# Optimization experiments

Measured on AMD Instinct MI355X. Metric: run time of the kernel, lower is better.

The kernel has to match this reference:

```python
import jax, jax.numpy as jnp
import numpy as np

EPS = 1e-5  # BatchNorm eps

def gcn_conv(x, src, dst, deg, dinv, W, b):
    # PyG GCNConv: out = D^{-1/2}(A+I)D^{-1/2} X W + b
    N = x.shape[0]
    xw = x @ W                               # [N, F_out]
    norm = dinv[src] * dinv[dst]             # [E]
    agg = jax.ops.segment_sum(xw[src] * norm[:, None], dst, num_segments=N)
    agg = agg + xw * (1.0 / deg)[:, None]    # self-loop term: deg^-1/2 * deg^-1/2
    return agg + b

def bn(x, g, b, m, v):
    # inference-mode BatchNorm1d over features
    return (x - m) * jax.lax.rsqrt(v + EPS) * g + b

def setup_inputs() -> dict:
    key = jax.random.key(0)
    N, E, F_in, C = 100000, 1600000, 128, 16
    dims = [F_in, 64, 128, 64, 32, C]
    ks = jax.random.split(key, 64)
    inp = {}
    inp["x"] = jax.random.normal(ks[0], (N, F_in), dtype=jnp.float32)
    inp["edge_index"] = jax.random.randint(ks[1], (2, E), 0, N, dtype=jnp.int32)
    ki = 2
    for l in range(5):
        fi, fo = dims[l], dims[l + 1]
        scale = 1.0 / np.sqrt(fi)
        inp[f"w{l+1}"] = jax.random.normal(ks[ki], (fi, fo), dtype=jnp.float32) * scale; ki += 1
        inp[f"b{l+1}"] = jnp.zeros((fo,), dtype=jnp.float32)
    for l in range(4):  # BN params for layers 1..4
        fo = dims[l + 1]
        inp[f"g{l+1}"] = jnp.ones((fo,), dtype=jnp.float32)
        inp[f"be{l+1}"] = jnp.zeros((fo,), dtype=jnp.float32)
        inp[f"m{l+1}"] = jax.random.normal(ks[ki], (fo,), dtype=jnp.float32) * 0.1; ki += 1
        inp[f"v{l+1}"] = jax.random.uniform(ks[ki], (fo,), dtype=jnp.float32, minval=0.5, maxval=1.5); ki += 1
    return inp

def reference(x, edge_index,
              w1, b1, w2, b2, w3, b3, w4, b4, w5, b5,
              g1, be1, m1, v1, g2, be2, m2, v2,
              g3, be3, m3, v3, g4, be4, m4, v4):
    N = x.shape[0]
    src, dst = edge_index[0], edge_index[1]
    deg = jax.ops.segment_sum(jnp.ones(src.shape[0], x.dtype), dst, num_segments=N) + 1.0
    dinv = jax.lax.rsqrt(deg)
    h = jax.nn.relu(bn(gcn_conv(x, src, dst, deg, dinv, w1, b1), g1, be1, m1, v1))
    h = jax.nn.relu(bn(gcn_conv(h, src, dst, deg, dinv, w2, b2), g2, be2, m2, v2))
    h = jax.nn.relu(bn(gcn_conv(h, src, dst, deg, dinv, w3, b3), g3, be3, m3, v3))
    h = jax.nn.relu(bn(gcn_conv(h, src, dst, deg, dinv, w4, b4), g4, be4, m4, v4))
    return gcn_conv(h, src, dst, deg, dinv, w5, b5)
```

## Files before the change

kernel.cpp:

```cpp
#include <hip/hip_runtime.h>
#include <hip/hip_fp16.h>

#define BEPS 1e-5f
static constexpr int TPB = 256;
static constexpr int G_SC = 512;
static constexpr int BK_SHIFT = 8;
static constexpr int BK_NODES = 256;
static constexpr int KMAX = 512;
static constexpr int BK_SLACK = 2048;

union F4H8 { float4 f4; __half2 h2[4]; };

typedef _Float16 half8 __attribute__((ext_vector_type(8)));
typedef float floatx4 __attribute__((ext_vector_type(4)));


__global__ __launch_bounds__(TPB) void k_zero_int(int* __restrict__ p, int n) {
  int i = blockIdx.x * TPB + threadIdx.x;
  if (i < n) p[i] = 0;
}

__global__ __launch_bounds__(TPB) void k_hist(const int* __restrict__ dst,
                                              int* __restrict__ histG,
                                              int* __restrict__ btot,
                                              int E, int K, int chunk) {
  __shared__ int lh[KMAX];
  int g = blockIdx.x, t = threadIdx.x;
  for (int i = t; i < KMAX; i += TPB) lh[i] = 0;
  __syncthreads();
  int e0 = g * chunk, e1 = min(E, e0 + chunk);
  for (int e = e0 + t * 4; e < e1; e += TPB * 4) {
    if (e + 4 <= e1) {
      int4 d4 = *reinterpret_cast<const int4*>(dst + e);
      atomicAdd(&lh[d4.x >> BK_SHIFT], 1);
      atomicAdd(&lh[d4.y >> BK_SHIFT], 1);
      atomicAdd(&lh[d4.z >> BK_SHIFT], 1);
      atomicAdd(&lh[d4.w >> BK_SHIFT], 1);
    } else {
      for (int q = e; q < e1; ++q) atomicAdd(&lh[dst[q] >> BK_SHIFT], 1);
    }
  }
  __syncthreads();
  for (int i = t; i < K; i += TPB) {
    histG[i * G_SC + g] = lh[i];
    atomicAdd(&btot[i], lh[i]);
  }
}

__global__ __launch_bounds__(KMAX) void k_bbase(const int* __restrict__ btot,
                                                int* __restrict__ bbase, int K) {
  __shared__ int sh[KMAX];
  int t = threadIdx.x;
  int v = (t < K) ? btot[t] : 0;
  sh[t] = v;
  __syncthreads();
  for (int s = 1; s < KMAX; s <<= 1) {
    int x = sh[t];
    int y = (t >= s) ? sh[t - s] : 0;
    __syncthreads();
    sh[t] = x + y;
    __syncthreads();
  }
  if (t < K) bbase[t] = sh[t] - v;
  if (t == 0) bbase[K] = sh[K - 1];
}

__global__ __launch_bounds__(G_SC) void k_offs(const int* __restrict__ histG,
                                               const int* __restrict__ bbase,
                                               int* __restrict__ offs) {
  __shared__ int sh[G_SC];
  int b = blockIdx.x, t = threadIdx.x;
  int v = histG[b * G_SC + t];
  sh[t] = v;
  __syncthreads();
  for (int s = 1; s < G_SC; s <<= 1) {
    int x = sh[t];
    int y = (t >= s) ? sh[t - s] : 0;
    __syncthreads();
    sh[t] = x + y;
    __syncthreads();
  }
  offs[b * G_SC + t] = bbase[b] + sh[t] - v;
}

__global__ __launch_bounds__(TPB) void k_scatter(const int* __restrict__ src,
                                                 const int* __restrict__ dst,
                                                 const int* __restrict__ offs,
                                                 unsigned int* __restrict__ pairs,
                                                 int E, int K, int chunk) {
  __shared__ int cur[KMAX];
  int g = blockIdx.x, t = threadIdx.x;
  for (int i = t; i < K; i += TPB) cur[i] = offs[i * G_SC + g];
  __syncthreads();
  int e0 = g * chunk, e1 = min(E, e0 + chunk);
  for (int e = e0 + t * 4; e < e1; e += TPB * 4) {
    if (e + 4 <= e1) {
      int4 d4 = *reinterpret_cast<const int4*>(dst + e);
      int4 s4 = *reinterpret_cast<const int4*>(src + e);
      int p0 = atomicAdd(&cur[d4.x >> BK_SHIFT], 1);
      pairs[p0] = (unsigned int)s4.x | ((unsigned int)(d4.x & (BK_NODES - 1)) << 20);
      int p1 = atomicAdd(&cur[d4.y >> BK_SHIFT], 1);
      pairs[p1] = (unsigned int)s4.y | ((unsigned int)(d4.y & (BK_NODES - 1)) << 20);
      int p2 = atomicAdd(&cur[d4.z >> BK_SHIFT], 1);
      pairs[p2] = (unsigned int)s4.z | ((unsigned int)(d4.z & (BK_NODES - 1)) << 20);
      int p3 = atomicAdd(&cur[d4.w >> BK_SHIFT], 1);
      pairs[p3] = (unsigned int)s4.w | ((unsigned int)(d4.w & (BK_NODES - 1)) << 20);
    } else {
      for (int q = e; q < e1; ++q) {
        int d = dst[q];
        int pos = atomicAdd(&cur[d >> BK_SHIFT], 1);
        pairs[pos] = (unsigned int)src[q] | ((unsigned int)(d & (BK_NODES - 1)) << 20);
      }
    }
  }
}

__global__ __launch_bounds__(TPB) void k_bucket_sort(const unsigned int* __restrict__ pairs,
                                                     const int* __restrict__ bbase,
                                                     int* __restrict__ rowptr,
                                                     int* __restrict__ rowend,
                                                     int* __restrict__ colidx,
                                                     float* __restrict__ dinv,
                                                     int N, int E) {
  __shared__ int cur[BK_NODES];
  __shared__ int sh[BK_NODES];
  int b = blockIdx.x, t = threadIdx.x;
  int base = bbase[b], end = bbase[b + 1];
  int n0 = b << BK_SHIFT;
  int nNodes = min(BK_NODES, N - n0);
  cur[t] = 0;
  __syncthreads();
  for (int e = base + t; e < end; e += TPB) atomicAdd(&cur[pairs[e] >> 20], 1);
  __syncthreads();
  int v = cur[t];
  int pd = (v + 7) & ~7;
  sh[t] = pd;
  __syncthreads();
  for (int s = 1; s < TPB; s <<= 1) {
    int x = sh[t];
    int y = (t >= s) ? sh[t - s] : 0;
    __syncthreads();
    sh[t] = x + y;
    __syncthreads();
  }
  int Bb = (base + b * BK_SLACK + 7) & ~7;
  int start = Bb + (sh[t] - pd);
  if (t < nNodes) {
    rowptr[n0 + t] = start;
    rowend[n0 + t] = start + pd;
    dinv[n0 + t] = rsqrtf((float)(v + 1));
    for (int i = start + v; i < start + pd; ++i) colidx[i] = N;
  }
  __syncthreads();
  cur[t] = start;
  __syncthreads();
  for (int e = base + t; e < end; e += TPB) {
    unsigned int p = pairs[e];
    int pos = atomicAdd(&cur[p >> 20], 1);
    colidx[pos] = (int)(p & 0xFFFFFu);
  }
}

__device__ inline void packone(const float* __restrict__ W, _Float16* __restrict__ Wp,
                               int i, int FO) {
  int j = i & 7, lane = (i >> 3) & 63, tile = i >> 9;
  int nct = FO >> 4, ct = tile % nct, kch = tile / nct;
  int k = kch * 32 + ((lane >> 4) << 3) + j;
  int n = (ct << 4) + (lane & 15);
  Wp[i] = (_Float16)W[k * FO + n];
}

__global__ __launch_bounds__(TPB) void k_packAll(const float* w1, _Float16* p1,
                                                 const float* w2, _Float16* p2,
                                                 const float* w3, _Float16* p3,
                                                 const float* w4, _Float16* p4,
                                                 const float* w5, _Float16* p5,
                                                 __half* bufA, int N) {
  int i = blockIdx.x * TPB + threadIdx.x;
  if (i < 8192) packone(w1, p1, i, 64);
  else if (i < 16384) packone(w2, p2, i - 8192, 128);
  else if (i < 24576) packone(w3, p3, i - 16384, 64);
  else if (i < 26624) packone(w4, p4, i - 24576, 32);
  else if (i < 27136) packone(w5, p5, i - 26624, 16);
  else if (i < 27144) {
    float4 z = {0.f, 0.f, 0.f, 0.f};
    reinterpret_cast<float4*>(bufA + (size_t)64 * N)[i - 27136] = z;
  }
}

template <int FI, int FO, int EPI, bool F32IN>
__global__ __launch_bounds__(TPB) void k_mgemm(const void* __restrict__ hin,
                                               const _Float16* __restrict__ Wp,
                                               const float* __restrict__ dinv,
                                               const float* __restrict__ bias,
                                               const float* __restrict__ g,
                                               const float* __restrict__ be,
                                               const float* __restrict__ m,
                                               const float* __restrict__ v,
                                               __half* __restrict__ out, int N) {
  constexpr int NCT = FO / 16;
  constexpr int NKC = FI / 32;
  __shared__ float4 Wsh[NKC * NCT * 64];
  for (int i = threadIdx.x; i < NKC * NCT * 64; i += TPB)
    Wsh[i] = reinterpret_cast<const float4*>(Wp)[i];
  __syncthreads();

  int lane = threadIdx.x & 63;
  int wv = threadIdx.x >> 6;
  int quad = lane >> 4;
  int rowBase = blockIdx.x * 64 + wv * 16;
  int rA = min(rowBase + (lane & 15), N - 1);

  floatx4 acc[NCT];
#pragma unroll
  for (int ct = 0; ct < NCT; ++ct) acc[ct] = (floatx4){0.f, 0.f, 0.f, 0.f};

#pragma unroll
  for (int kch = 0; kch < NKC; ++kch) {
    half8 a;
    if constexpr (F32IN) {
      const float4* xp = reinterpret_cast<const float4*>(hin);
      size_t idx = ((size_t)rA * FI + kch * 32 + quad * 8) >> 2;
      float4 fa = xp[idx], fb = xp[idx + 1];
      a[0] = (_Float16)fa.x; a[1] = (_Float16)fa.y; a[2] = (_Float16)fa.z; a[3] = (_Float16)fa.w;
      a[4] = (_Float16)fb.x; a[5] = (_Float16)fb.y; a[6] = (_Float16)fb.z; a[7] = (_Float16)fb.w;
    } else {
      union { float4 f4; half8 h8; } ua;
      ua.f4 = reinterpret_cast<const float4*>(hin)[((size_t)rA * FI + kch * 32 + quad * 8) >> 3];
      a = ua.h8;
    }
#pragma unroll
    for (int ct = 0; ct < NCT; ++ct) {
      union { float4 f4; half8 h8; } ub;
      ub.f4 = Wsh[(kch * NCT + ct) * 64 + lane];
      acc[ct] = __builtin_amdgcn_mfma_f32_16x16x32_f16(a, ub.h8, acc[ct], 0, 0, 0);
    }
  }

  int r0 = rowBase + quad * 4;
  float dv[4];
#pragma unroll
  for (int reg = 0; reg < 4; ++reg) dv[reg] = (r0 + reg < N) ? dinv[r0 + reg] : 0.f;
#pragma unroll
  for (int ct = 0; ct < NCT; ++ct) {
    int col = ct * 16 + (lane & 15);
#pragma unroll
    for (int reg = 0; reg < 4; ++reg) {
      int r = r0 + reg;
      out[(size_t)r * FO + col] = __float2half(acc[ct][reg] * dv[reg]);
    }
  }
  (void)bias; (void)g; (void)be; (void)m; (void)v;
}

template <int DO_BN>
__device__ inline void agg_gather64(const float4* __restrict__ in16,
                                    const int* __restrict__ rowptr,
                                    const int* __restrict__ rowend,
                                    const int* __restrict__ colidx,
                                    const float* __restrict__ dinv,
                                    const float* __restrict__ b_,
                                    const float* __restrict__ g_,
                                    const float* __restrict__ be_,
                                    const float* __restrict__ m_,
                                    const float* __restrict__ v_,
                                    int node, int quad, int N, half8 afr[2]) {
  bool valid = node < N;
  int rd = valid ? node : N;
  int e0 = valid ? rowptr[node] : 0;
  int e1 = valid ? rowend[node] : 0;
  float acc[2][8];
#pragma unroll
  for (int kch = 0; kch < 2; ++kch) {
    F4H8 u;
    u.f4 = in16[(size_t)rd * 8 + kch * 4 + quad];
#pragma unroll
    for (int i = 0; i < 4; ++i) {
      float2 t2 = __half22float2(u.h2[i]);
      acc[kch][2 * i] = t2.x;
      acc[kch][2 * i + 1] = t2.y;
    }
  }
  for (int e = e0; e < e1; e += 4) {
    int4 c = *reinterpret_cast<const int4*>(colidx + e);
#pragma unroll
    for (int kch = 0; kch < 2; ++kch) {
      int g = kch * 4 + quad;
      F4H8 u0, u1, u2, u3;
      u0.f4 = in16[(size_t)c.x * 8 + g];
      u1.f4 = in16[(size_t)c.y * 8 + g];
      u2.f4 = in16[(size_t)c.z * 8 + g];
      u3.f4 = in16[(size_t)c.w * 8 + g];
#pragma unroll
      for (int i = 0; i < 4; ++i) {
        float2 a = __half22float2(u0.h2[i]), b = __half22float2(u1.h2[i]);
        float2 cc = __half22float2(u2.h2[i]), d = __half22float2(u3.h2[i]);
        acc[kch][2 * i] += (a.x + b.x) + (cc.x + d.x);
        acc[kch][2 * i + 1] += (a.y + b.y) + (cc.y + d.y);
      }
    }
  }
  float dv = valid ? dinv[node] : 0.f;
#pragma unroll
  for (int kch = 0; kch < 2; ++kch) {
    int f0 = kch * 32 + quad * 8;
#pragma unroll
    for (int j = 0; j < 8; ++j) {
      float val = acc[kch][j] * dv;
      if (DO_BN) {
        int f = f0 + j;
        float sc = g_[f] * rsqrtf(v_[f] + BEPS);
        val = fmaxf((val + b_[f] - m_[f]) * sc + be_[f], 0.f);
      }
      afr[kch][j] = (_Float16)val;
    }
  }
}

__global__ __launch_bounds__(TPB) void k_aggemm23(const __half* __restrict__ hin,
                                                  const int* __restrict__ rowptr,
                                                  const int* __restrict__ rowend,
                                                  const int* __restrict__ colidx,
                                                  const _Float16* __restrict__ W2p,
                                                  const _Float16* __restrict__ W3p,
                                                  const float* __restrict__ dinv,
                                                  const float* __restrict__ b2,
                                                  const float* __restrict__ g2,
                                                  const float* __restrict__ be2,
                                                  const float* __restrict__ m2,
                                                  const float* __restrict__ v2,
                                                  __half* __restrict__ out, int N) {
  __shared__ float4 W2s[2 * 8 * 64];
  __shared__ float4 W3s[4 * 4 * 64];
  __shared__ _Float16 tr[4 * 16 * 136];
  for (int i = threadIdx.x; i < 1024; i += TPB) W2s[i] = reinterpret_cast<const float4*>(W2p)[i];
  for (int i = threadIdx.x; i < 1024; i += TPB) W3s[i] = reinterpret_cast<const float4*>(W3p)[i];
  __syncthreads();

  int lane = threadIdx.x & 63;
  int wv = threadIdx.x >> 6;
  int quad = lane >> 4;
  int m = lane & 15;
  int rowBase = blockIdx.x * 64 + wv * 16;

  half8 afr[2];
  agg_gather64<0>(reinterpret_cast<const float4*>(hin), rowptr, rowend, colidx, dinv,
                  nullptr, nullptr, nullptr, nullptr, nullptr, rowBase + m, quad, N, afr);

  floatx4 acc1[8];
#pragma unroll
  for (int ct = 0; ct < 8; ++ct) acc1[ct] = (floatx4){0.f, 0.f, 0.f, 0.f};
#pragma unroll
  for (int kch = 0; kch < 2; ++kch) {
#pragma unroll
    for (int ct = 0; ct < 8; ++ct) {
      union { float4 f4; half8 h8; } ub;
      ub.f4 = W2s[(kch * 8 + ct) * 64 + lane];
      acc1[ct] = __builtin_amdgcn_mfma_f32_16x16x32_f16(afr[kch], ub.h8, acc1[ct], 0, 0, 0);
    }
  }
  _Float16* mytr = tr + wv * 16 * 136;
#pragma unroll
  for (int ct = 0; ct < 8; ++ct) {
    int col = ct * 16 + m;
    float sc = g2[col] * rsqrtf(v2[col] + BEPS);
    float bb = b2[col] - m2[col];
    float ee = be2[col];
#pragma unroll
    for (int reg = 0; reg < 4; ++reg) {
      int r = quad * 4 + reg;
      mytr[r * 136 + col] = (_Float16)fmaxf((acc1[ct][reg] + bb) * sc + ee, 0.f);
    }
  }
  floatx4 acc2[4];
#pragma unroll
  for (int ct = 0; ct < 4; ++ct) acc2[ct] = (floatx4){0.f, 0.f, 0.f, 0.f};
#pragma unroll
  for (int kch = 0; kch < 4; ++kch) {
    half8 a2 = *reinterpret_cast<const half8*>(&mytr[m * 136 + kch * 32 + quad * 8]);
#pragma unroll
    for (int ct = 0; ct < 4; ++ct) {
      union { float4 f4; half8 h8; } ub;
      ub.f4 = W3s[(kch * 4 + ct) * 64 + lane];
      acc2[ct] = __builtin_amdgcn_mfma_f32_16x16x32_f16(a2, ub.h8, acc2[ct], 0, 0, 0);
    }
  }
  int r0 = rowBase + quad * 4;
  float dv[4];
#pragma unroll
  for (int reg = 0; reg < 4; ++reg) dv[reg] = (r0 + reg < N) ? dinv[r0 + reg] : 0.f;
#pragma unroll
  for (int ct = 0; ct < 4; ++ct) {
    int col = ct * 16 + m;
#pragma unroll
    for (int reg = 0; reg < 4; ++reg) {
      int r = r0 + reg;
      out[(size_t)r * 64 + col] = __float2half(acc2[ct][reg] * dv[reg]);
    }
  }
}

template <int FO>
__global__ __launch_bounds__(TPB) void k_aggemm64(const __half* __restrict__ hin,
                                                  const int* __restrict__ rowptr,
                                                  const int* __restrict__ rowend,
                                                  const int* __restrict__ colidx,
                                                  const _Float16* __restrict__ Wp,
                                                  const float* __restrict__ dinv,
                                                  const float* __restrict__ b_,
                                                  const float* __restrict__ g_,
                                                  const float* __restrict__ be_,
                                                  const float* __restrict__ m_,
                                                  const float* __restrict__ v_,
                                                  __half* __restrict__ out, int N) {
  constexpr int NCT = FO / 16;
  __shared__ float4 Wsh[2 * NCT * 64];
  for (int i = threadIdx.x; i < 2 * NCT * 64; i += TPB)
    Wsh[i] = reinterpret_cast<const float4*>(Wp)[i];
  __syncthreads();

  int lane = threadIdx.x & 63;
  int wv = threadIdx.x >> 6;
  int quad = lane >> 4;
  int m = lane & 15;
  int rowBase = blockIdx.x * 64 + wv * 16;

  half8 afr[2];
  agg_gather64<1>(reinterpret_cast<const float4*>(hin), rowptr, rowend, colidx, dinv,
                  b_, g_, be_, m_, v_, rowBase + m, quad, N, afr);

  floatx4 acc[NCT];
#pragma unroll
  for (int ct = 0; ct < NCT; ++ct) acc[ct] = (floatx4){0.f, 0.f, 0.f, 0.f};
#pragma unroll
  for (int kch = 0; kch < 2; ++kch) {
#pragma unroll
    for (int ct = 0; ct < NCT; ++ct) {
      union { float4 f4; half8 h8; } ub;
      ub.f4 = Wsh[(kch * NCT + ct) * 64 + lane];
      acc[ct] = __builtin_amdgcn_mfma_f32_16x16x32_f16(afr[kch], ub.h8, acc[ct], 0, 0, 0);
    }
  }
  int r0 = rowBase + quad * 4;
  float dv[4];
#pragma unroll
  for (int reg = 0; reg < 4; ++reg) dv[reg] = (r0 + reg < N) ? dinv[r0 + reg] : 0.f;
#pragma unroll
  for (int ct = 0; ct < NCT; ++ct) {
    int col = ct * 16 + m;
#pragma unroll
    for (int reg = 0; reg < 4; ++reg) {
      int r = r0 + reg;
      out[(size_t)r * FO + col] = __float2half(acc[ct][reg] * dv[reg]);
    }
  }
}

__global__ __launch_bounds__(TPB) void k_aggemm5(const __half* __restrict__ hin,
                                                 const int* __restrict__ rowptr,
                                                 const int* __restrict__ rowend,
                                                 const int* __restrict__ colidx,
                                                 const _Float16* __restrict__ Wp,
                                                 const float* __restrict__ dinv,
                                                 const float* __restrict__ b_,
                                                 const float* __restrict__ g_,
                                                 const float* __restrict__ be_,
                                                 const float* __restrict__ m_,
                                                 const float* __restrict__ v_,
                                                 __half* __restrict__ out, int N) {
  __shared__ float4 Wsh[64];
  if (threadIdx.x < 64) Wsh[threadIdx.x] = reinterpret_cast<const float4*>(Wp)[threadIdx.x];
  __syncthreads();

  int lane = threadIdx.x & 63;
  int wv = threadIdx.x >> 6;
  int quad = lane >> 4;
  int m = lane & 15;
  int rowBase = blockIdx.x * 64 + wv * 16;
  int node = rowBase + m;
  bool valid = node < N;
  int rd = valid ? node : N;
  int e0 = valid ? rowptr[node] : 0;
  int e1 = valid ? rowend[node] : 0;
  const float4* in16 = reinterpret_cast<const float4*>(hin);

  float acc[8];
  {
    F4H8 u;
    u.f4 = in16[(size_t)rd * 4 + quad];
#pragma unroll
    for (int i = 0; i < 4; ++i) {
      float2 t2 = __half22float2(u.h2[i]);
      acc[2 * i] = t2.x;
      acc[2 * i + 1] = t2.y;
    }
  }
  for (int e = e0; e < e1; e += 4) {
    int4 c = *reinterpret_cast<const int4*>(colidx + e);
    F4H8 u0, u1, u2, u3;
    u0.f4 = in16[(size_t)c.x * 4 + quad];
    u1.f4 = in16[(size_t)c.y * 4 + quad];
    u2.f4 = in16[(size_t)c.z * 4 + quad];
    u3.f4 = in16[(size_t)c.w * 4 + quad];
#pragma unroll
    for (int i = 0; i < 4; ++i) {
      float2 a = __half22float2(u0.h2[i]), b = __half22float2(u1.h2[i]);
      float2 cc = __half22float2(u2.h2[i]), d = __half22float2(u3.h2[i]);
      acc[2 * i] += (a.x + b.x) + (cc.x + d.x);
      acc[2 * i + 1] += (a.y + b.y) + (cc.y + d.y);
    }
  }
  float dvn = valid ? dinv[node] : 0.f;
  half8 afr;
#pragma unroll
  for (int j = 0; j < 8; ++j) {
    int f = quad * 8 + j;
    float sc = g_[f] * rsqrtf(v_[f] + BEPS);
    float val = fmaxf((acc[j] * dvn + b_[f] - m_[f]) * sc + be_[f], 0.f);
    afr[j] = (_Float16)val;
  }
  floatx4 c0 = (floatx4){0.f, 0.f, 0.f, 0.f};
  union { float4 f4; half8 h8; } ub;
  ub.f4 = Wsh[lane];
  c0 = __builtin_amdgcn_mfma_f32_16x16x32_f16(afr, ub.h8, c0, 0, 0, 0);
  int r0 = rowBase + quad * 4;
#pragma unroll
  for (int reg = 0; reg < 4; ++reg) {
    int r = r0 + reg;
    float dv = (r < N) ? dinv[r] : 0.f;
    out[(size_t)r * 16 + m] = __float2half(c0[reg] * dv);
  }
}

template <int F, int MODE, typename TO>
__global__ __launch_bounds__(TPB) void k_agg(const __half* __restrict__ in,
                                             const int* __restrict__ rowptr,
                                             const int* __restrict__ rowend,
                                             const int* __restrict__ colidx,
                                             const float* __restrict__ dinv,
                                             const float* __restrict__ bias,
                                             const float* __restrict__ g,
                                             const float* __restrict__ be,
                                             const float* __restrict__ m,
                                             const float* __restrict__ v,
                                             TO* __restrict__ out, int N) {
  constexpr int V = F / 8;
  constexpr int NPB = TPB / V;
  int node = blockIdx.x * NPB + (int)(threadIdx.x / V);
  int lane = threadIdx.x % V;
  if (node >= N) return;
  const float4* in16 = reinterpret_cast<const float4*>(in);
  const size_t rs = F / 8;
  float acc[8];
  {
    F4H8 u;
    u.f4 = in16[(size_t)node * rs + lane];
#pragma unroll
    for (int i = 0; i < 4; ++i) {
      float2 t2 = __half22float2(u.h2[i]);
      acc[2 * i] = t2.x;
      acc[2 * i + 1] = t2.y;
    }
  }
  int e0 = rowptr[node], e1 = rowend[node];
  int e = e0;
  for (; e + 8 <= e1; e += 8) {
    int4 c0 = *reinterpret_cast<const int4*>(colidx + e);
    int4 c1 = *reinterpret_cast<const int4*>(colidx + e + 4);
    F4H8 u[8];
    u[0].f4 = in16[(size_t)c0.x * rs + lane];
    u[1].f4 = in16[(size_t)c0.y * rs + lane];
    u[2].f4 = in16[(size_t)c0.z * rs + lane];
    u[3].f4 = in16[(size_t)c0.w * rs + lane];
    u[4].f4 = in16[(size_t)c1.x * rs + lane];
    u[5].f4 = in16[(size_t)c1.y * rs + lane];
    u[6].f4 = in16[(size_t)c1.z * rs + lane];
    u[7].f4 = in16[(size_t)c1.w * rs + lane];
#pragma unroll
    for (int q = 0; q < 8; ++q) {
#pragma unroll
      for (int i = 0; i < 4; ++i) {
        float2 t2 = __half22float2(u[q].h2[i]);
        acc[2 * i] += t2.x;
        acc[2 * i + 1] += t2.y;
      }
    }
  }
  float dv = dinv[node];
#pragma unroll
  for (int i = 0; i < 8; ++i) acc[i] *= dv;
  if (MODE == 0) {
    float4 ba = reinterpret_cast<const float4*>(bias)[lane * 2];
    float4 bb = reinterpret_cast<const float4*>(bias)[lane * 2 + 1];
    acc[0] += ba.x; acc[1] += ba.y; acc[2] += ba.z; acc[3] += ba.w;
    acc[4] += bb.x; acc[5] += bb.y; acc[6] += bb.z; acc[7] += bb.w;
  } else if (MODE == 1 || MODE == 2) {
    const float4* B = reinterpret_cast<const float4*>(bias);
    const float4* G = reinterpret_cast<const float4*>(g);
    const float4* Be = reinterpret_cast<const float4*>(be);
    const float4* M = reinterpret_cast<const float4*>(m);
    const float4* Vv = reinterpret_cast<const float4*>(v);
#pragma unroll
    for (int h = 0; h < 2; ++h) {
      float4 b4 = B[lane * 2 + h], g4 = G[lane * 2 + h], e4 = Be[lane * 2 + h];
      float4 m4 = M[lane * 2 + h], v4 = Vv[lane * 2 + h];
      float* a = acc + 4 * h;
      a[0] = fmaxf((a[0] + b4.x - m4.x) * (g4.x * rsqrtf(v4.x + BEPS)) + e4.x, 0.f);
      a[1] = fmaxf((a[1] + b4.y - m4.y) * (g4.y * rsqrtf(v4.y + BEPS)) + e4.y, 0.f);
      a[2] = fmaxf((a[2] + b4.z - m4.z) * (g4.z * rsqrtf(v4.z + BEPS)) + e4.z, 0.f);
      a[3] = fmaxf((a[3] + b4.w - m4.w) * (g4.w * rsqrtf(v4.w + BEPS)) + e4.w, 0.f);
    }
    if (MODE == 2) {
#pragma unroll
      for (int i = 0; i < 8; ++i) acc[i] *= dv;
    }
  }
  if constexpr (sizeof(TO) == 2) {
    F4H8 u;
#pragma unroll
    for (int i = 0; i < 4; ++i) u.h2[i] = __floats2half2_rn(acc[2 * i], acc[2 * i + 1]);
    reinterpret_cast<float4*>(out)[(size_t)node * rs + lane] = u.f4;
  } else {
    float4 o0 = {acc[0], acc[1], acc[2], acc[3]};
    float4 o1 = {acc[4], acc[5], acc[6], acc[7]};
    float4* op = reinterpret_cast<float4*>((float*)out + (size_t)node * F + lane * 8);
    op[0] = o0;
    op[1] = o1;
  }
}


extern "C" void kernel_launch(void* const* d_in, const int* in_sizes, int n_in,
                              void* d_out, int out_size, void* d_ws, size_t ws_size,
                              hipStream_t stream) {
  const float* x = (const float*)d_in[0];
  const int* ei = (const int*)d_in[1];
  const int N = in_sizes[0] / 128;
  const int E = in_sizes[1] / 2;
  const int* src = ei;
  const int* dst = ei + E;

  const float* w1 = (const float*)d_in[2];  const float* b1 = (const float*)d_in[3];
  const float* w2 = (const float*)d_in[4];  const float* b2 = (const float*)d_in[5];
  const float* w3 = (const float*)d_in[6];  const float* b3 = (const float*)d_in[7];
  const float* w4 = (const float*)d_in[8];  const float* b4 = (const float*)d_in[9];
  const float* w5 = (const float*)d_in[10]; const float* b5 = (const float*)d_in[11];
  const float* g1 = (const float*)d_in[12]; const float* be1 = (const float*)d_in[13];
  const float* m1 = (const float*)d_in[14]; const float* v1 = (const float*)d_in[15];
  const float* g2 = (const float*)d_in[16]; const float* be2 = (const float*)d_in[17];
  const float* m2 = (const float*)d_in[18]; const float* v2 = (const float*)d_in[19];
  const float* g3 = (const float*)d_in[20]; const float* be3 = (const float*)d_in[21];
  const float* m3 = (const float*)d_in[22]; const float* v3 = (const float*)d_in[23];
  const float* g4 = (const float*)d_in[24]; const float* be4 = (const float*)d_in[25];
  const float* m4 = (const float*)d_in[26]; const float* v4 = (const float*)d_in[27];
  float* out = (float*)d_out;

  char* ws = (char*)d_ws;
  size_t off = 0;
  auto alloc = [&](size_t bytes) -> void* {
    void* p = ws + off;
    off += (bytes + 255) & ~(size_t)255;
    return p;
  };
  const int K = (N + BK_NODES - 1) >> BK_SHIFT;
  float*        dinv   = (float*)alloc((size_t)N * 4);
  int*          rowptr = (int*)alloc((size_t)N * 4);
  int*          rowend = (int*)alloc((size_t)N * 4);
  int*          colidx = (int*)alloc(((size_t)E + (size_t)(K + 1) * BK_SLACK) * 4);
  unsigned int* pairs  = (unsigned int*)alloc((size_t)E * 4);
  int*          histG  = (int*)alloc((size_t)KMAX * G_SC * 4);
  int*          offs   = (int*)alloc((size_t)KMAX * G_SC * 4);
  int*          btot   = (int*)alloc(KMAX * 4);
  int*          bbase  = (int*)alloc((KMAX + 1) * 4);
  _Float16*     wp1    = (_Float16*)alloc(128 * 64 * 2);
  _Float16*     wp2    = (_Float16*)alloc(64 * 128 * 2);
  _Float16*     wp3    = (_Float16*)alloc(128 * 64 * 2);
  _Float16*     wp4    = (_Float16*)alloc(64 * 32 * 2);
  _Float16*     wp5    = (_Float16*)alloc(32 * 16 * 2);
  __half*       bufA   = (__half*)alloc((size_t)(N + 64) * 128 * 2);
  __half*       bufB   = (__half*)alloc((size_t)(N + 64) * 128 * 2);
  (void)ws_size; (void)n_in; (void)out_size;

  const int chunk = (((E + G_SC - 1) / G_SC) + 3) & ~3;

  k_zero_int<<<2, TPB, 0, stream>>>(btot, KMAX);
  k_hist<<<G_SC, TPB, 0, stream>>>(dst, histG, btot, E, K, chunk);
  k_bbase<<<1, KMAX, 0, stream>>>(btot, bbase, K);
  k_offs<<<K, G_SC, 0, stream>>>(histG, bbase, offs);
  k_scatter<<<G_SC, TPB, 0, stream>>>(src, dst, offs, pairs, E, K, chunk);
  k_bucket_sort<<<K, TPB, 0, stream>>>(pairs, bbase, rowptr, rowend, colidx, dinv, N, E);

  k_packAll<<<(27144 + TPB - 1) / TPB, TPB, 0, stream>>>(w1, wp1, w2, wp2, w3, wp3, w4, wp4, w5, wp5, bufA, N);

  int gRow = (N + 63) / 64;
  k_mgemm<128, 64, 0, true><<<gRow, TPB, 0, stream>>>(x, wp1, dinv, nullptr, nullptr, nullptr, nullptr, nullptr, bufB, N);
  k_agg<64, 2, __half><<<(N + 31) / 32, TPB, 0, stream>>>(bufB, rowptr, rowend, colidx, dinv, b1, g1, be1, m1, v1, bufA, N);
  k_aggemm23<<<gRow, TPB, 0, stream>>>(bufA, rowptr, rowend, colidx, wp2, wp3, dinv, b2, g2, be2, m2, v2, bufB, N);
  k_aggemm64<32><<<gRow, TPB, 0, stream>>>(bufB, rowptr, rowend, colidx, wp4, dinv, b3, g3, be3, m3, v3, bufA, N);
  k_aggemm5<<<gRow, TPB, 0, stream>>>(bufA, rowptr, rowend, colidx, wp5, dinv, b4, g4, be4, m4, v4, bufB, N);
  k_agg<16, 0, float><<<(N + 127) / 128, TPB, 0, stream>>>(bufB, rowptr, rowend, colidx, dinv, b5, nullptr, nullptr, nullptr, nullptr, out, N);
}
```

Before: 364.3 us.

## Split fused aggregate-GEMM kernels into separate gather and MFMA GEMM kernels

```diff
diff --git a/kernel.cpp b/kernel.cpp
--- a/kernel.cpp
+++ b/kernel.cpp
@@ -188,15 +188,63 @@
   }
 }
 
-template <int FI, int FO, int EPI, bool F32IN>
-__global__ __launch_bounds__(TPB) void k_mgemm(const void* __restrict__ hin,
+__global__ __launch_bounds__(TPB) void k_mgemm1(const float* __restrict__ x,
+                                                const _Float16* __restrict__ Wp,
+                                                const float* __restrict__ dinv,
+                                                __half* __restrict__ out, int N) {
+  __shared__ float4 Wsh[4 * 4 * 64];
+  __shared__ _Float16 xs[64 * 136];
+  for (int i = threadIdx.x; i < 1024; i += TPB)
+    Wsh[i] = reinterpret_cast<const float4*>(Wp)[i];
+  int rowBase = blockIdx.x * 64;
+  for (int i = threadIdx.x; i < 2048; i += TPB) {
+    int r = i >> 5, c4 = i & 31;
+    int gr = rowBase + r;
+    float4 f = {0.f, 0.f, 0.f, 0.f};
+    if (gr < N) f = reinterpret_cast<const float4*>(x)[(size_t)gr * 32 + c4];
+    _Float16* p = &xs[r * 136 + c4 * 4];
+    p[0] = (_Float16)f.x; p[1] = (_Float16)f.y; p[2] = (_Float16)f.z; p[3] = (_Float16)f.w;
+  }
+  __syncthreads();
+
+  int lane = threadIdx.x & 63;
+  int wv = threadIdx.x >> 6;
+  int quad = lane >> 4;
+  int m = lane & 15;
+  int lrow = wv * 16 + m;
+
+  floatx4 acc[4];
+#pragma unroll
+  for (int ct = 0; ct < 4; ++ct) acc[ct] = (floatx4){0.f, 0.f, 0.f, 0.f};
+#pragma unroll
+  for (int kch = 0; kch < 4; ++kch) {
+    half8 a = *reinterpret_cast<const half8*>(&xs[lrow * 136 + kch * 32 + quad * 8]);
+#pragma unroll
+    for (int ct = 0; ct < 4; ++ct) {
+      union { float4 f4; half8 h8; } ub;
+      ub.f4 = Wsh[(kch * 4 + ct) * 64 + lane];
+      acc[ct] = __builtin_amdgcn_mfma_f32_16x16x32_f16(a, ub.h8, acc[ct], 0, 0, 0);
+    }
+  }
+  int r0 = rowBase + wv * 16 + quad * 4;
+  float dv[4];
+#pragma unroll
+  for (int reg = 0; reg < 4; ++reg) dv[reg] = (r0 + reg < N) ? dinv[r0 + reg] : 0.f;
+#pragma unroll
+  for (int ct = 0; ct < 4; ++ct) {
+    int col = ct * 16 + m;
+#pragma unroll
+    for (int reg = 0; reg < 4; ++reg) {
+      int r = r0 + reg;
+      out[(size_t)r * 64 + col] = __float2half(acc[ct][reg] * dv[reg]);
+    }
+  }
+}
+
+template <int FI, int FO>
+__global__ __launch_bounds__(TPB) void k_mgemm(const __half* __restrict__ hin,
                                                const _Float16* __restrict__ Wp,
                                                const float* __restrict__ dinv,
-                                               const float* __restrict__ bias,
-                                               const float* __restrict__ g,
-                                               const float* __restrict__ be,
-                                               const float* __restrict__ m,
-                                               const float* __restrict__ v,
                                                __half* __restrict__ out, int N) {
   constexpr int NCT = FO / 16;
   constexpr int NKC = FI / 32;
@@ -214,29 +262,17 @@
   floatx4 acc[NCT];
 #pragma unroll
   for (int ct = 0; ct < NCT; ++ct) acc[ct] = (floatx4){0.f, 0.f, 0.f, 0.f};
-
 #pragma unroll
   for (int kch = 0; kch < NKC; ++kch) {
-    half8 a;
-    if constexpr (F32IN) {
-      const float4* xp = reinterpret_cast<const float4*>(hin);
-      size_t idx = ((size_t)rA * FI + kch * 32 + quad * 8) >> 2;
-      float4 fa = xp[idx], fb = xp[idx + 1];
-      a[0] = (_Float16)fa.x; a[1] = (_Float16)fa.y; a[2] = (_Float16)fa.z; a[3] = (_Float16)fa.w;
-      a[4] = (_Float16)fb.x; a[5] = (_Float16)fb.y; a[6] = (_Float16)fb.z; a[7] = (_Float16)fb.w;
-    } else {
-      union { float4 f4; half8 h8; } ua;
-      ua.f4 = reinterpret_cast<const float4*>(hin)[((size_t)rA * FI + kch * 32 + quad * 8) >> 3];
-      a = ua.h8;
-    }
+    union { float4 f4; half8 h8; } ua;
+    ua.f4 = reinterpret_cast<const float4*>(hin)[((size_t)rA * FI + kch * 32 + quad * 8) >> 3];
 #pragma unroll
     for (int ct = 0; ct < NCT; ++ct) {
       union { float4 f4; half8 h8; } ub;
       ub.f4 = Wsh[(kch * NCT + ct) * 64 + lane];
-      acc[ct] = __builtin_amdgcn_mfma_f32_16x16x32_f16(a, ub.h8, acc[ct], 0, 0, 0);
-    }
-  }
-
+      acc[ct] = __builtin_amdgcn_mfma_f32_16x16x32_f16(ua.h8, ub.h8, acc[ct], 0, 0, 0);
+    }
+  }
   int r0 = rowBase + quad * 4;
   float dv[4];
 #pragma unroll
@@ -250,86 +286,18 @@
       out[(size_t)r * FO + col] = __float2half(acc[ct][reg] * dv[reg]);
     }
   }
-  (void)bias; (void)g; (void)be; (void)m; (void)v;
-}
-
-template <int DO_BN>
-__device__ inline void agg_gather64(const float4* __restrict__ in16,
-                                    const int* __restrict__ rowptr,
-                                    const int* __restrict__ rowend,
-                                    const int* __restrict__ colidx,
-                                    const float* __restrict__ dinv,
-                                    const float* __restrict__ b_,
-                                    const float* __restrict__ g_,
-                                    const float* __restrict__ be_,
-                                    const float* __restrict__ m_,
-                                    const float* __restrict__ v_,
-                                    int node, int quad, int N, half8 afr[2]) {
-  bool valid = node < N;
-  int rd = valid ? node : N;
-  int e0 = valid ? rowptr[node] : 0;
-  int e1 = valid ? rowend[node] : 0;
-  float acc[2][8];
-#pragma unroll
-  for (int kch = 0; kch < 2; ++kch) {
-    F4H8 u;
-    u.f4 = in16[(size_t)rd * 8 + kch * 4 + quad];
-#pragma unroll
-    for (int i = 0; i < 4; ++i) {
-      float2 t2 = __half22float2(u.h2[i]);
-      acc[kch][2 * i] = t2.x;
-      acc[kch][2 * i + 1] = t2.y;
-    }
-  }
-  for (int e = e0; e < e1; e += 4) {
-    int4 c = *reinterpret_cast<const int4*>(colidx + e);
-#pragma unroll
-    for (int kch = 0; kch < 2; ++kch) {
-      int g = kch * 4 + quad;
-      F4H8 u0, u1, u2, u3;
-      u0.f4 = in16[(size_t)c.x * 8 + g];
-      u1.f4 = in16[(size_t)c.y * 8 + g];
-      u2.f4 = in16[(size_t)c.z * 8 + g];
-      u3.f4 = in16[(size_t)c.w * 8 + g];
-#pragma unroll
-      for (int i = 0; i < 4; ++i) {
-        float2 a = __half22float2(u0.h2[i]), b = __half22float2(u1.h2[i]);
-        float2 cc = __half22float2(u2.h2[i]), d = __half22float2(u3.h2[i]);
-        acc[kch][2 * i] += (a.x + b.x) + (cc.x + d.x);
-        acc[kch][2 * i + 1] += (a.y + b.y) + (cc.y + d.y);
-      }
-    }
-  }
-  float dv = valid ? dinv[node] : 0.f;
-#pragma unroll
-  for (int kch = 0; kch < 2; ++kch) {
-    int f0 = kch * 32 + quad * 8;
-#pragma unroll
-    for (int j = 0; j < 8; ++j) {
-      float val = acc[kch][j] * dv;
-      if (DO_BN) {
-        int f = f0 + j;
-        float sc = g_[f] * rsqrtf(v_[f] + BEPS);
-        val = fmaxf((val + b_[f] - m_[f]) * sc + be_[f], 0.f);
-      }
-      afr[kch][j] = (_Float16)val;
-    }
-  }
-}
-
-__global__ __launch_bounds__(TPB) void k_aggemm23(const __half* __restrict__ hin,
-                                                  const int* __restrict__ rowptr,
-                                                  const int* __restrict__ rowend,
-                                                  const int* __restrict__ colidx,
-                                                  const _Float16* __restrict__ W2p,
-                                                  const _Float16* __restrict__ W3p,
-                                                  const float* __restrict__ dinv,
-                                                  const float* __restrict__ b2,
-                                                  const float* __restrict__ g2,
-                                                  const float* __restrict__ be2,
-                                                  const float* __restrict__ m2,
-                                                  const float* __restrict__ v2,
-                                                  __half* __restrict__ out, int N) {
+}
+
+__global__ __launch_bounds__(TPB) void k_mgemm23(const __half* __restrict__ hin,
+                                                 const _Float16* __restrict__ W2p,
+                                                 const _Float16* __restrict__ W3p,
+                                                 const float* __restrict__ dinv,
+                                                 const float* __restrict__ b2,
+                                                 const float* __restrict__ g2,
+                                                 const float* __restrict__ be2,
+                                                 const float* __restrict__ m2,
+                                                 const float* __restrict__ v2,
+                                                 __half* __restrict__ out, int N) {
   __shared__ float4 W2s[2 * 8 * 64];
   __shared__ float4 W3s[4 * 4 * 64];
   __shared__ _Float16 tr[4 * 16 * 136];
@@ -342,21 +310,20 @@
   int quad = lane >> 4;
   int m = lane & 15;
   int rowBase = blockIdx.x * 64 + wv * 16;
-
-  half8 afr[2];
-  agg_gather64<0>(reinterpret_cast<const float4*>(hin), rowptr, rowend, colidx, dinv,
-                  nullptr, nullptr, nullptr, nullptr, nullptr, rowBase + m, quad, N, afr);
+  int rA = min(rowBase + m, N - 1);
 
   floatx4 acc1[8];
 #pragma unroll
   for (int ct = 0; ct < 8; ++ct) acc1[ct] = (floatx4){0.f, 0.f, 0.f, 0.f};
 #pragma unroll
   for (int kch = 0; kch < 2; ++kch) {
+    union { float4 f4; half8 h8; } ua;
+    ua.f4 = reinterpret_cast<const float4*>(hin)[((size_t)rA * 64 + kch * 32 + quad * 8) >> 3];
 #pragma unroll
     for (int ct = 0; ct < 8; ++ct) {
       union { float4 f4; half8 h8; } ub;
       ub.f4 = W2s[(kch * 8 + ct) * 64 + lane];
-      acc1[ct] = __builtin_amdgcn_mfma_f32_16x16x32_f16(afr[kch], ub.h8, acc1[ct], 0, 0, 0);
+      acc1[ct] = __builtin_amdgcn_mfma_f32_16x16x32_f16(ua.h8, ub.h8, acc1[ct], 0, 0, 0);
     }
   }
   _Float16* mytr = tr + wv * 16 * 136;
@@ -396,62 +363,6 @@
     for (int reg = 0; reg < 4; ++reg) {
       int r = r0 + reg;
       out[(size_t)r * 64 + col] = __float2half(acc2[ct][reg] * dv[reg]);
-    }
-  }
-}
-
-template <int FO>
-__global__ __launch_bounds__(TPB) void k_aggemm64(const __half* __restrict__ hin,
-                                                  const int* __restrict__ rowptr,
-                                                  const int* __restrict__ rowend,
-                                                  const int* __restrict__ colidx,
-                                                  const _Float16* __restrict__ Wp,
-                                                  const float* __restrict__ dinv,
-                                                  const float* __restrict__ b_,
-                                                  const float* __restrict__ g_,
-                                                  const float* __restrict__ be_,
-                                                  const float* __restrict__ m_,
-                                                  const float* __restrict__ v_,
-                                                  __half* __restrict__ out, int N) {
-  constexpr int NCT = FO / 16;
-  __shared__ float4 Wsh[2 * NCT * 64];
-  for (int i = threadIdx.x; i < 2 * NCT * 64; i += TPB)
-    Wsh[i] = reinterpret_cast<const float4*>(Wp)[i];
-  __syncthreads();
-
-  int lane = threadIdx.x & 63;
-  int wv = threadIdx.x >> 6;
-  int quad = lane >> 4;
-  int m = lane & 15;
-  int rowBase = blockIdx.x * 64 + wv * 16;
-
-  half8 afr[2];
-  agg_gather64<1>(reinterpret_cast<const float4*>(hin), rowptr, rowend, colidx, dinv,
-                  b_, g_, be_, m_, v_, rowBase + m, quad, N, afr);
-
-  floatx4 acc[NCT];
-#pragma unroll
-  for (int ct = 0; ct < NCT; ++ct) acc[ct] = (floatx4){0.f, 0.f, 0.f, 0.f};
-#pragma unroll
-  for (int kch = 0; kch < 2; ++kch) {
-#pragma unroll
-    for (int ct = 0; ct < NCT; ++ct) {
-      union { float4 f4; half8 h8; } ub;
-      ub.f4 = Wsh[(kch * NCT + ct) * 64 + lane];
-      acc[ct] = __builtin_amdgcn_mfma_f32_16x16x32_f16(afr[kch], ub.h8, acc[ct], 0, 0, 0);
-    }
-  }
-  int r0 = rowBase + quad * 4;
-  float dv[4];
-#pragma unroll
-  for (int reg = 0; reg < 4; ++reg) dv[reg] = (r0 + reg < N) ? dinv[r0 + reg] : 0.f;
-#pragma unroll
-  for (int ct = 0; ct < NCT; ++ct) {
-    int col = ct * 16 + m;
-#pragma unroll
-    for (int reg = 0; reg < 4; ++reg) {
-      int r = r0 + reg;
-      out[(size_t)r * FO + col] = __float2half(acc[ct][reg] * dv[reg]);
     }
   }
 }
@@ -564,7 +475,39 @@
   }
   int e0 = rowptr[node], e1 = rowend[node];
   int e = e0;
-  for (; e + 8 <= e1; e += 8) {
+  for (; e + 16 <= e1; e += 16) {
+    int4 c0 = *reinterpret_cast<const int4*>(colidx + e);
+    int4 c1 = *reinterpret_cast<const int4*>(colidx + e + 4);
+    int4 c2 = *reinterpret_cast<const int4*>(colidx + e + 8);
+    int4 c3 = *reinterpret_cast<const int4*>(colidx + e + 12);
+    F4H8 u[16];
+    u[0].f4  = in16[(size_t)c0.x * rs + lane];
+    u[1].f4  = in16[(size_t)c0.y * rs + lane];
+    u[2].f4  = in16[(size_t)c0.z * rs + lane];
+    u[3].f4  = in16[(size_t)c0.w * rs + lane];
+    u[4].f4  = in16[(size_t)c1.x * rs + lane];
+    u[5].f4  = in16[(size_t)c1.y * rs + lane];
+    u[6].f4  = in16[(size_t)c1.z * rs + lane];
+    u[7].f4  = in16[(size_t)c1.w * rs + lane];
+    u[8].f4  = in16[(size_t)c2.x * rs + lane];
+    u[9].f4  = in16[(size_t)c2.y * rs + lane];
+    u[10].f4 = in16[(size_t)c2.z * rs + lane];
+    u[11].f4 = in16[(size_t)c2.w * rs + lane];
+    u[12].f4 = in16[(size_t)c3.x * rs + lane];
+    u[13].f4 = in16[(size_t)c3.y * rs + lane];
+    u[14].f4 = in16[(size_t)c3.z * rs + lane];
+    u[15].f4 = in16[(size_t)c3.w * rs + lane];
+#pragma unroll
+    for (int q = 0; q < 16; ++q) {
+#pragma unroll
+      for (int i = 0; i < 4; ++i) {
+        float2 t2 = __half22float2(u[q].h2[i]);
+        acc[2 * i] += t2.x;
+        acc[2 * i + 1] += t2.y;
+      }
+    }
+  }
+  if (e < e1) {
     int4 c0 = *reinterpret_cast<const int4*>(colidx + e);
     int4 c1 = *reinterpret_cast<const int4*>(colidx + e + 4);
     F4H8 u[8];
@@ -693,10 +636,12 @@
   k_packAll<<<(27144 + TPB - 1) / TPB, TPB, 0, stream>>>(w1, wp1, w2, wp2, w3, wp3, w4, wp4, w5, wp5, bufA, N);
 
   int gRow = (N + 63) / 64;
-  k_mgemm<128, 64, 0, true><<<gRow, TPB, 0, stream>>>(x, wp1, dinv, nullptr, nullptr, nullptr, nullptr, nullptr, bufB, N);
+  k_mgemm1<<<gRow, TPB, 0, stream>>>(x, wp1, dinv, bufB, N);
   k_agg<64, 2, __half><<<(N + 31) / 32, TPB, 0, stream>>>(bufB, rowptr, rowend, colidx, dinv, b1, g1, be1, m1, v1, bufA, N);
-  k_aggemm23<<<gRow, TPB, 0, stream>>>(bufA, rowptr, rowend, colidx, wp2, wp3, dinv, b2, g2, be2, m2, v2, bufB, N);
-  k_aggemm64<32><<<gRow, TPB, 0, stream>>>(bufB, rowptr, rowend, colidx, wp4, dinv, b3, g3, be3, m3, v3, bufA, N);
+  k_agg<64, 3, __half><<<(N + 31) / 32, TPB, 0, stream>>>(bufA, rowptr, rowend, colidx, dinv, nullptr, nullptr, nullptr, nullptr, nullptr, bufB, N);
+  k_mgemm23<<<gRow, TPB, 0, stream>>>(bufB, wp2, wp3, dinv, b2, g2, be2, m2, v2, bufA, N);
+  k_agg<64, 1, __half><<<(N + 31) / 32, TPB, 0, stream>>>(bufA, rowptr, rowend, colidx, dinv, b3, g3, be3, m3, v3, bufB, N);
+  k_mgemm<64, 32><<<gRow, TPB, 0, stream>>>(bufB, wp4, dinv, bufA, N);
   k_aggemm5<<<gRow, TPB, 0, stream>>>(bufA, rowptr, rowend, colidx, wp5, dinv, b4, g4, be4, m4, v4, bufB, N);
   k_agg<16, 0, float><<<(N + 127) / 128, TPB, 0, stream>>>(bufB, rowptr, rowend, colidx, dinv, b5, nullptr, nullptr, nullptr, nullptr, out, N);
 }
```

Result: faster. 357.1 us (-2.0%).
